# Kernel tuning notes

Hardware: AMD Instinct MI355X
Metric: run time of the kernel (lower is better)

Reference implementation:

```python
import jax, jax.numpy as jnp
import numpy as np

MAX_ITERS = 50
EPS_NORM = 1e-8
EPS_SEP = -1e-6


def setup_inputs() -> dict:
    key = jax.random.key(0)
    k1, k2 = jax.random.split(key)
    pointcloud = jax.random.normal(k1, (200000, 3), dtype=jnp.float32)
    targets = jax.random.normal(k2, (256, 3), dtype=jnp.float32)
    return {"pointcloud": pointcloud, "targets": targets}


def reference(pointcloud, targets):
    # pointcloud: [N, d], targets: [M, d]
    N = pointcloud.shape[0]
    M = targets.shape[0]
    p2 = jnp.sum(pointcloud * pointcloud, axis=1)  # [N]
    t2 = jnp.sum(targets * targets, axis=1)        # [M]

    def step(mask, _):
        # squared euclidean distances [M, N] (argmin identical to cdist argmin)
        d2 = t2[:, None] + p2[None, :] - 2.0 * (targets @ pointcloud.T)
        d2 = jnp.where(mask, d2, jnp.inf)
        closest_idx = jnp.argmin(d2, axis=1)           # [M]
        closest_points = pointcloud[closest_idx]       # [M, d]
        a = closest_points - targets
        a = a / (jnp.linalg.norm(a, axis=1, keepdims=True) + EPS_NORM)
        b = jnp.sum(a * closest_points, axis=1)        # [M]
        dot = a @ pointcloud.T - b[:, None]            # [M, N]
        separated = dot >= EPS_SEP
        mask = mask & ~separated
        return mask, (a, b)

    mask0 = jnp.ones((M, N), dtype=bool)
    _, (a_stack, b_stack) = jax.lax.scan(step, mask0, None, length=MAX_ITERS)
    return a_stack, b_stack  # [MAX_ITERS, M, d], [MAX_ITERS, M]
```

## Files before the change

### kernel.cpp

```cpp
#include <hip/hip_runtime.h>
#include <stdint.h>
#include <math.h>

#pragma clang fp contract(off)

#define BLOCK 1024
#define NW (BLOCK / 64)
#define PT 8
#define PB 4
#define MAX_ITERS 50
#define SOLO_CAP 2048
#define EPS_NORM 1e-8f
#define EPS_SEP (-1e-6f)

__global__ __launch_bounds__(BLOCK) void convex_plane_kernel(
    const float* __restrict__ pc, const float* __restrict__ tg,
    float* __restrict__ out, int N, int M, int CAP, int stepsA)
{
    extern __shared__ uint32_t smem[];
    const int tid  = threadIdx.x;
    const int lane = tid & 63;
    const int wv   = tid >> 6;
    const int m    = blockIdx.x;

    const int maskW = stepsA * (PT * BLOCK / 32);
    uint32_t* mask  = smem;
    int*      list  = (int*)(smem + maskW);
    float*    red_d = (float*)(list + CAP);
    int*      red_i = (int*)(red_d + NW);
    int*      cw    = red_i + NW;
    int*      bcast = cw + NW;
    int*      cnt   = bcast + 2;

    const float tx = tg[3*m+0], ty = tg[3*m+1], tz = tg[3*m+2];
    const float t2 = tx*tx + ty*ty + tz*tz;

    float* out_a = out;
    float* out_b = out + (size_t)MAX_ITERS * (size_t)M * 3;

    auto finish = [&](float dmin, int imin, int mycnt, bool cntFromCursor) -> int2 {
        #pragma unroll
        for (int off = 32; off > 0; off >>= 1) {
            float od = __shfl_down(dmin, off, 64);
            int   oi = __shfl_down(imin, off, 64);
            int   oc = __shfl_down(mycnt, off, 64);
            if (od < dmin || (od == dmin && oi < imin)) { dmin = od; imin = oi; }
            mycnt += oc;
        }
        if (lane == 0) { red_d[wv] = dmin; red_i[wv] = imin; cw[wv] = mycnt; }
        __syncthreads();
        if (wv == 0) {
            float bd = (lane < NW) ? red_d[lane] : INFINITY;
            int   bi = (lane < NW) ? red_i[lane] : 0;
            int   c  = (lane < NW) ? cw[lane]    : 0;
            #pragma unroll
            for (int off = 8; off > 0; off >>= 1) {
                float od = __shfl_down(bd, off, 64);
                int   oi = __shfl_down(bi, off, 64);
                int   oc = __shfl_down(c,  off, 64);
                if (od < bd || (od == bd && oi < bi)) { bd = od; bi = oi; }
                c += oc;
            }
            if (lane == 0) { bcast[0] = bi; bcast[1] = cntFromCursor ? cnt[0] : c; }
        }
        __syncthreads();
        int2 r; r.x = bcast[0]; r.y = bcast[1];
        return r;
    };

    auto scanA = [&](int mode, bool build,
                     float ax, float ay, float az, float b) -> int2 {
        if (tid == 0) cnt[0] = 0;
        __syncthreads();
        float dmin = INFINITY;
        int   imin = 0;
        int   mycnt = 0;
        for (int s = 0; s < stepsA; ++s) {
            const int ib    = s * PT * BLOCK + tid;
            const int wbase = s * (PT * BLOCK / 32);
            uint32_t live = 0;
            if (mode == 2) {
                #pragma unroll
                for (int j = 0; j < PT; ++j) {
                    uint32_t w = mask[wbase + j * (BLOCK / 32) + (tid >> 5)];
                    live |= ((w >> (tid & 31)) & 1u) << j;
                }
            } else {
                #pragma unroll
                for (int j = 0; j < PT; ++j)
                    if (ib + j * BLOCK < N) live |= (1u << j);
            }
            float px[PT], py[PT], pz[PT];
            #pragma unroll
            for (int j = 0; j < PT; ++j) {
                if ((live >> j) & 1u) {
                    const float* p = pc + 3 * (size_t)(ib + j * BLOCK);
                    px[j] = p[0]; py[j] = p[1]; pz[j] = p[2];
                }
            }
            uint32_t keepm = 0;
            #pragma unroll
            for (int j = 0; j < PT; ++j) {
                if ((live >> j) & 1u) {
                    bool keep;
                    if (mode == 0) keep = true;
                    else {
                        float dt = ax*px[j] + ay*py[j] + az*pz[j] - b;
                        keep = (dt < EPS_SEP);
                    }
                    if (keep) {
                        keepm |= (1u << j);
                        float p2 = px[j]*px[j] + py[j]*py[j] + pz[j]*pz[j];
                        float tp = tx*px[j] + ty*py[j] + tz*pz[j];
                        float d2 = t2 + p2 - 2.0f*tp;
                        if (d2 < dmin) { dmin = d2; imin = ib + j * BLOCK; }
                    }
                }
            }
            if (mode != 0) {
                #pragma unroll
                for (int j = 0; j < PT; ++j) {
                    unsigned long long bal = __ballot(((keepm >> j) & 1u) != 0u);
                    const int widx = wbase + j * (BLOCK / 32) + (wv << 1);
                    if (lane == 0)       mask[widx]     = (uint32_t)bal;
                    else if (lane == 32) mask[widx + 1] = (uint32_t)(bal >> 32);
                }
            }
            mycnt += (int)__popc(keepm);
            if (build) {
                int c = (int)__popc(keepm);
                int incl = c;
                #pragma unroll
                for (int off = 1; off < 64; off <<= 1) {
                    int o = __shfl_up(incl, off, 64);
                    if (lane >= off) incl += o;
                }
                const int excl = incl - c;
                const int tot  = __shfl(incl, 63, 64);
                int wb = 0;
                if (lane == 0) wb = atomicAdd(cnt, tot);
                wb = __shfl(wb, 0, 64);
                int pos = wb + excl;
                #pragma unroll
                for (int j = 0; j < PT; ++j) {
                    if ((keepm >> j) & 1u) {
                        if (pos < CAP) list[pos] = ib + j * BLOCK;
                        ++pos;
                    }
                }
            }
        }
        return finish(dmin, imin, mycnt, false);
    };

    auto scanB = [&](int count, float ax, float ay, float az, float b) -> int2 {
        if (tid == 0) cnt[0] = 0;
        __syncthreads();
        float dmin = INFINITY;
        int   imin = 0;
        const int per = BLOCK * PB;
        const int bsteps = (count + per - 1) / per;
        for (int s = 0; s < bsteps; ++s) {
            int jv[PB]; float d2v[PB];
            uint32_t keepm = 0;
            #pragma unroll
            for (int q = 0; q < PB; ++q) {
                const int e = s * per + q * BLOCK + tid;
                if (e < count) {
                    const int j = list[e];
                    jv[q] = j;
                    const float* p = pc + 3 * (size_t)j;
                    float px = p[0], py = p[1], pz = p[2];
                    float dt = ax*px + ay*py + az*pz - b;
                    if (dt < EPS_SEP) {
                        keepm |= (1u << q);
                        float p2 = px*px + py*py + pz*pz;
                        float tp = tx*px + ty*py + tz*pz;
                        d2v[q] = t2 + p2 - 2.0f*tp;
                    }
                }
            }
            __syncthreads();
            int c = (int)__popc(keepm);
            int incl = c;
            #pragma unroll
            for (int off = 1; off < 64; off <<= 1) {
                int o = __shfl_up(incl, off, 64);
                if (lane >= off) incl += o;
            }
            const int excl = incl - c;
            const int tot  = __shfl(incl, 63, 64);
            int wb = 0;
            if (lane == 0) wb = atomicAdd(cnt, tot);
            wb = __shfl(wb, 0, 64);
            int pos = wb + excl;
            #pragma unroll
            for (int q = 0; q < PB; ++q) {
                if ((keepm >> q) & 1u) {
                    list[pos] = jv[q];
                    if (d2v[q] < dmin || (d2v[q] == dmin && jv[q] < imin)) {
                        dmin = d2v[q]; imin = jv[q];
                    }
                    ++pos;
                }
            }
        }
        __syncthreads();
        return finish(dmin, imin, 0, true);
    };

    bool comp = false;
    int2 rc = scanA(0, false, 0.f, 0.f, 0.f, 0.f);
    int idx = rc.x, count = rc.y;

    for (int k = 0; k < MAX_ITERS; ++k) {
        if (comp && count <= SOLO_CAP) {
            if (wv != 0) return;
            for (; k < MAX_ITERS; ++k) {
                const float cx = pc[3*idx+0], cy = pc[3*idx+1], cz = pc[3*idx+2];
                const float vx = cx - tx, vy = cy - ty, vz = cz - tz;
                const float nrm = sqrtf(vx*vx + vy*vy + vz*vz);
                const float den = nrm + EPS_NORM;
                const float ax = vx / den, ay = vy / den, az = vz / den;
                const float b  = ax*cx + ay*cy + az*cz;
                if (count == 0) {
                    for (int q = lane; q < MAX_ITERS - k; q += 64) {
                        const int kk = k + q;
                        const size_t oa = ((size_t)kk * M + m) * 3;
                        out_a[oa+0] = ax; out_a[oa+1] = ay; out_a[oa+2] = az;
                        out_b[(size_t)kk * M + m] = b;
                    }
                    return;
                }
                if (lane == 0) {
                    const size_t oa = ((size_t)k * M + m) * 3;
                    out_a[oa+0] = ax; out_a[oa+1] = ay; out_a[oa+2] = az;
                    out_b[(size_t)k * M + m] = b;
                }
                if (k + 1 < MAX_ITERS) {
                    float dmin = INFINITY; int imin = 0; int wcur = 0;
                    for (int e0 = 0; e0 < count; e0 += 64) {
                        const int e = e0 + lane;
                        bool keep = false; int j = 0; float d2v = 0.f;
                        if (e < count) {
                            j = list[e];
                            const float* p = pc + 3 * (size_t)j;
                            float px = p[0], py = p[1], pz = p[2];
                            float dt = ax*px + ay*py + az*pz - b;
                            if (dt < EPS_SEP) {
                                keep = true;
                                float p2 = px*px + py*py + pz*pz;
                                float tp = tx*px + ty*py + tz*pz;
                                d2v = t2 + p2 - 2.0f*tp;
                            }
                        }
                        unsigned long long bal = __ballot(keep);
                        int pos = wcur + (int)__popcll(bal & ((1ull << lane) - 1ull));
                        if (keep) {
                            list[pos] = j;
                            if (d2v < dmin || (d2v == dmin && j < imin)) {
                                dmin = d2v; imin = j;
                            }
                        }
                        wcur += (int)__popcll(bal);
                    }
                    #pragma unroll
                    for (int off = 32; off > 0; off >>= 1) {
                        float od = __shfl_down(dmin, off, 64);
                        int   oi = __shfl_down(imin, off, 64);
                        if (od < dmin || (od == dmin && oi < imin)) { dmin = od; imin = oi; }
                    }
                    idx = __shfl(imin, 0, 64);
                    count = wcur;
                }
            }
            return;
        }

        const float cx = pc[3*idx+0], cy = pc[3*idx+1], cz = pc[3*idx+2];
        const float vx = cx - tx, vy = cy - ty, vz = cz - tz;
        const float nrm = sqrtf(vx*vx + vy*vy + vz*vz);
        const float den = nrm + EPS_NORM;
        const float ax = vx / den, ay = vy / den, az = vz / den;
        const float b  = ax*cx + ay*cy + az*cz;

        if (count == 0) {
            for (int q = tid; q < MAX_ITERS - k; q += BLOCK) {
                const int kk = k + q;
                const size_t oa = ((size_t)kk * M + m) * 3;
                out_a[oa+0] = ax; out_a[oa+1] = ay; out_a[oa+2] = az;
                out_b[(size_t)kk * M + m] = b;
            }
            return;
        }
        if (tid == 0) {
            const size_t oa = ((size_t)k * M + m) * 3;
            out_a[oa+0] = ax; out_a[oa+1] = ay; out_a[oa+2] = az;
            out_b[(size_t)k * M + m] = b;
        }
        if (k + 1 < MAX_ITERS) {
            if (comp) {
                rc = scanB(count, ax, ay, az, b);
            } else {
                const bool build = (count <= 2 * CAP);
                rc = scanA(k == 0 ? 1 : 2, build, ax, ay, az, b);
                if (build && rc.y <= CAP) comp = true;
            }
            idx = rc.x; count = rc.y;
        }
    }
}

extern "C" void kernel_launch(void* const* d_in, const int* in_sizes, int n_in,
                              void* d_out, int out_size, void* d_ws, size_t ws_size,
                              hipStream_t stream) {
    const float* pc = (const float*)d_in[0];
    const float* tg = (const float*)d_in[1];
    float* out = (float*)d_out;
    const int N = in_sizes[0] / 3;
    const int M = in_sizes[1] / 3;
    const int stepsA = (N + BLOCK * PT - 1) / (BLOCK * PT);
    const size_t maskB  = (size_t)stepsA * (PT * BLOCK / 32) * sizeof(uint32_t);
    const size_t fixedB = NW * (2 * sizeof(int) + sizeof(float)) + 3 * sizeof(int);

    int CAP = 32768;
    size_t smem = maskB + (size_t)CAP * sizeof(int) + fixedB;
    if (hipFuncSetAttribute((const void*)convex_plane_kernel,
                            hipFuncAttributeMaxDynamicSharedMemorySize,
                            (int)smem) != hipSuccess) {
        CAP = 8192;
        smem = maskB + (size_t)CAP * sizeof(int) + fixedB;
    }
    convex_plane_kernel<<<M, BLOCK, smem, stream>>>(pc, tg, out, N, M, CAP, stepsA);
}
```

Baseline: 595.8 us.

## Stage surviving points as float4 records in LDS for the single-wave tail

Before the single-wave tail phase, the whole block copies each surviving point's coordinates and index into a float4 record in shared memory. The wave then compacts and scans these records instead of gathering coordinates from global memory through an index list. The loop is unrolled four-way, and the winning point's coordinates travel with the argmin reduction, so the next plane no longer needs a global load. The cost is four times more shared memory per list entry, plus an extra block-wide copy and two barriers on entry.

```diff
diff --git a/kernel.cpp b/kernel.cpp
--- a/kernel.cpp
+++ b/kernel.cpp
@@ -215,15 +215,32 @@
 
     for (int k = 0; k < MAX_ITERS; ++k) {
         if (comp && count <= SOLO_CAP) {
+            int myj[2]; int nm = 0;
+            for (int e = tid; e < count; e += BLOCK) myj[nm++] = list[e];
+            __syncthreads();
+            nm = 0;
+            for (int e = tid; e < count; e += BLOCK) {
+                const int j = myj[nm++];
+                const float* p = pc + 3 * (size_t)j;
+                float4 r; r.x = p[0]; r.y = p[1]; r.z = p[2];
+                r.w = __int_as_float(j);
+                ((float4*)list)[e] = r;
+            }
+            __syncthreads();
             if (wv != 0) return;
+            float4* rec = (float4*)list;
+
+            float ccx, ccy, ccz;
+            { const float* p = pc + 3 * (size_t)idx; ccx = p[0]; ccy = p[1]; ccz = p[2]; }
+
             for (; k < MAX_ITERS; ++k) {
-                const float cx = pc[3*idx+0], cy = pc[3*idx+1], cz = pc[3*idx+2];
-                const float vx = cx - tx, vy = cy - ty, vz = cz - tz;
-                const float nrm = sqrtf(vx*vx + vy*vy + vz*vz);
-                const float den = nrm + EPS_NORM;
-                const float ax = vx / den, ay = vy / den, az = vz / den;
-                const float b  = ax*cx + ay*cy + az*cz;
                 if (count == 0) {
+                    const float c0 = pc[0], c1 = pc[1], c2 = pc[2];
+                    const float vx = c0 - tx, vy = c1 - ty, vz = c2 - tz;
+                    const float nrm = sqrtf(vx*vx + vy*vy + vz*vz);
+                    const float den = nrm + EPS_NORM;
+                    const float ax = vx / den, ay = vy / den, az = vz / den;
+                    const float b  = ax*c0 + ay*c1 + az*c2;
                     for (int q = lane; q < MAX_ITERS - k; q += 64) {
                         const int kk = k + q;
                         const size_t oa = ((size_t)kk * M + m) * 3;
@@ -232,45 +249,66 @@
                     }
                     return;
                 }
+                const float vx = ccx - tx, vy = ccy - ty, vz = ccz - tz;
+                const float nrm = sqrtf(vx*vx + vy*vy + vz*vz);
+                const float den = nrm + EPS_NORM;
+                const float ax = vx / den, ay = vy / den, az = vz / den;
+                const float b  = ax*ccx + ay*ccy + az*ccz;
                 if (lane == 0) {
                     const size_t oa = ((size_t)k * M + m) * 3;
                     out_a[oa+0] = ax; out_a[oa+1] = ay; out_a[oa+2] = az;
                     out_b[(size_t)k * M + m] = b;
                 }
                 if (k + 1 < MAX_ITERS) {
-                    float dmin = INFINITY; int imin = 0; int wcur = 0;
-                    for (int e0 = 0; e0 < count; e0 += 64) {
-                        const int e = e0 + lane;
-                        bool keep = false; int j = 0; float d2v = 0.f;
-                        if (e < count) {
-                            j = list[e];
-                            const float* p = pc + 3 * (size_t)j;
-                            float px = p[0], py = p[1], pz = p[2];
-                            float dt = ax*px + ay*py + az*pz - b;
-                            if (dt < EPS_SEP) {
-                                keep = true;
-                                float p2 = px*px + py*py + pz*pz;
-                                float tp = tx*px + ty*py + tz*pz;
-                                d2v = t2 + p2 - 2.0f*tp;
+                    float dmin = INFINITY; int imin = 0;
+                    float mx = 0.f, my = 0.f, mz = 0.f;
+                    int wcur = 0;
+                    for (int g0 = 0; g0 < count; g0 += 256) {
+                        float4 r[4]; float dv[4];
+                        uint32_t km = 0;
+                        #pragma unroll
+                        for (int u = 0; u < 4; ++u) {
+                            const int e = g0 + u * 64 + lane;
+                            if (e < count) {
+                                r[u] = rec[e];
+                                float dt = ax*r[u].x + ay*r[u].y + az*r[u].z - b;
+                                if (dt < EPS_SEP) {
+                                    km |= (1u << u);
+                                    float p2 = r[u].x*r[u].x + r[u].y*r[u].y + r[u].z*r[u].z;
+                                    float tp = tx*r[u].x + ty*r[u].y + tz*r[u].z;
+                                    dv[u] = t2 + p2 - 2.0f*tp;
+                                }
                             }
                         }
-                        unsigned long long bal = __ballot(keep);
-                        int pos = wcur + (int)__popcll(bal & ((1ull << lane) - 1ull));
-                        if (keep) {
-                            list[pos] = j;
-                            if (d2v < dmin || (d2v == dmin && j < imin)) {
-                                dmin = d2v; imin = j;
+                        #pragma unroll
+                        for (int u = 0; u < 4; ++u) {
+                            unsigned long long bal = __ballot(((km >> u) & 1u) != 0u);
+                            int pos = wcur + (int)__popcll(bal & ((1ull << lane) - 1ull));
+                            if ((km >> u) & 1u) {
+                                rec[pos] = r[u];
+                                const int j = __float_as_int(r[u].w);
+                                if (dv[u] < dmin || (dv[u] == dmin && j < imin)) {
+                                    dmin = dv[u]; imin = j;
+                                    mx = r[u].x; my = r[u].y; mz = r[u].z;
+                                }
                             }
+                            wcur += (int)__popcll(bal);
                         }
-                        wcur += (int)__popcll(bal);
                     }
                     #pragma unroll
                     for (int off = 32; off > 0; off >>= 1) {
                         float od = __shfl_down(dmin, off, 64);
                         int   oi = __shfl_down(imin, off, 64);
-                        if (od < dmin || (od == dmin && oi < imin)) { dmin = od; imin = oi; }
-                    }
-                    idx = __shfl(imin, 0, 64);
+                        float ox = __shfl_down(mx, off, 64);
+                        float oy = __shfl_down(my, off, 64);
+                        float oz = __shfl_down(mz, off, 64);
+                        if (od < dmin || (od == dmin && oi < imin)) {
+                            dmin = od; imin = oi; mx = ox; my = oy; mz = oz;
+                        }
+                    }
+                    ccx = __shfl(mx, 0, 64);
+                    ccy = __shfl(my, 0, 64);
+                    ccz = __shfl(mz, 0, 64);
                     count = wcur;
                 }
             }
```

After: 598.7 us. Within noise of the previous version (+0.5%).
